# Optimization experiments

Measured on AMD Instinct MI355X. Metric: run time of the kernel, lower is better.

The kernel has to match this reference:

```python
import jax, jax.numpy as jnp
import numpy as np

B, H, W, C = 16, 64, 64, 192
NH, WS, SHIFT = 6, 8, 4          # heads, window size, shift (window//2)
DEPTH, MLP_R = 2, 4
N = WS * WS                      # tokens per window = 64
HD = C // NH                     # head dim = 32
SCALE = HD ** -0.5
TBL = (2 * WS - 1) ** 2          # relative-bias table size = 225
NW = (H // WS) * (W // WS)       # windows per image = 64


def _rel_pos_index():
    coords = np.stack(np.meshgrid(np.arange(WS), np.arange(WS), indexing='ij')).reshape(2, -1)
    rel = (coords[:, :, None] - coords[:, None, :]).transpose(1, 2, 0)
    rel[..., 0] += WS - 1
    rel[..., 1] += WS - 1
    rel[..., 0] *= 2 * WS - 1
    return jnp.asarray(rel.sum(-1))  # [N, N] int


def _attn_mask():
    # Swin shifted-window mask: region ids then pairwise -100 where ids differ.
    img = np.zeros((H, W))
    sl = (slice(0, -WS), slice(-WS, -SHIFT), slice(-SHIFT, None))
    cnt = 0
    for hs in sl:
        for ws in sl:
            img[hs, ws] = cnt
            cnt += 1
    mw = img.reshape(H // WS, WS, W // WS, WS).transpose(0, 2, 1, 3).reshape(-1, N)
    diff = mw[:, None, :] - mw[:, :, None]
    return jnp.asarray(np.where(diff != 0, -100.0, 0.0).astype(np.float32))  # [NW, N, N]


REL_IDX = _rel_pos_index()
ATTN_MASK = _attn_mask()


def _ln(x, g, b, eps=1e-5):
    mu = x.mean(-1, keepdims=True)
    var = ((x - mu) ** 2).mean(-1, keepdims=True)
    return (x - mu) * jax.lax.rsqrt(var + eps) * g + b


def setup_inputs() -> dict:
    key = jax.random.key(0)
    ks = jax.random.split(key, 8)
    s = 0.02
    return {
        'x': jax.random.normal(ks[0], (B, H * W, C), jnp.float32),
        'norm1_g': jnp.ones((DEPTH, C)), 'norm1_b': jnp.zeros((DEPTH, C)),
        'qkv_w': jax.random.normal(ks[1], (DEPTH, 3 * C, C)) * s,
        'qkv_b': jnp.zeros((DEPTH, 3 * C)),
        'bias_table': jax.random.normal(ks[2], (DEPTH, TBL, NH)) * s,
        'proj_w': jax.random.normal(ks[3], (DEPTH, C, C)) * s,
        'proj_b': jnp.zeros((DEPTH, C)),
        'norm2_g': jnp.ones((DEPTH, C)), 'norm2_b': jnp.zeros((DEPTH, C)),
        'fc1_w': jax.random.normal(ks[4], (DEPTH, MLP_R * C, C)) * s,
        'fc1_b': jnp.zeros((DEPTH, MLP_R * C)),
        'fc2_w': jax.random.normal(ks[5], (DEPTH, C, MLP_R * C)) * s,
        'fc2_b': jnp.zeros((DEPTH, C)),
    }


def _block(x, shift, n1g, n1b, qw, qb, tbl, pw, pb, n2g, n2b, f1w, f1b, f2w, f2b):
    shortcut = x
    y = _ln(x, n1g, n1b).reshape(B, H, W, C)
    if shift > 0:
        y = jnp.roll(y, (-shift, -shift), axis=(1, 2))
    # window partition -> [B*NW, N, C]
    win = y.reshape(B, H // WS, WS, W // WS, WS, C).transpose(0, 1, 3, 2, 4, 5).reshape(-1, N, C)
    qkv = (win @ qw.T + qb).reshape(-1, N, 3, NH, HD).transpose(2, 0, 3, 1, 4)
    q, k, v = qkv[0] * SCALE, qkv[1], qkv[2]          # each [B*NW, NH, N, HD]
    attn = jnp.einsum('bhnd,bhmd->bhnm', q, k)
    attn = attn + tbl[REL_IDX].transpose(2, 0, 1)[None]  # relative position bias
    if shift > 0:
        attn = (attn.reshape(B, NW, NH, N, N) + ATTN_MASK[None, :, None]).reshape(-1, NH, N, N)
    attn = jax.nn.softmax(attn, axis=-1)
    o = jnp.einsum('bhnm,bhmd->bhnd', attn, v).transpose(0, 2, 1, 3).reshape(-1, N, C)
    o = o @ pw.T + pb
    # window reverse
    y = o.reshape(B, H // WS, W // WS, WS, WS, C).transpose(0, 1, 3, 2, 4, 5).reshape(B, H, W, C)
    if shift > 0:
        y = jnp.roll(y, (shift, shift), axis=(1, 2))
    x = shortcut + y.reshape(B, H * W, C)
    h = _ln(x, n2g, n2b)
    h = jax.nn.gelu(h @ f1w.T + f1b, approximate=False)  # torch nn.GELU = exact erf
    return x + (h @ f2w.T + f2b)


def reference(x, norm1_g, norm1_b, qkv_w, qkv_b, bias_table, proj_w, proj_b,
              norm2_g, norm2_b, fc1_w, fc1_b, fc2_w, fc2_b):
    for i in range(DEPTH):
        shift = 0 if i % 2 == 0 else SHIFT
        x = _block(x, shift, norm1_g[i], norm1_b[i], qkv_w[i], qkv_b[i], bias_table[i],
                   proj_w[i], proj_b[i], norm2_g[i], norm2_b[i],
                   fc1_w[i], fc1_b[i], fc2_w[i], fc2_b[i])
    return x
```

## Files before the change

### kernel.cpp

```cpp
#include <hip/hip_runtime.h>
#include <hip/hip_bf16.h>
#include <math.h>

typedef __hip_bfloat16 bf16;
typedef short bf16x8 __attribute__((ext_vector_type(8)));
typedef short s16x4 __attribute__((ext_vector_type(4)));
typedef float f32x4 __attribute__((ext_vector_type(4)));

#define TOKENS 65536
#define C_ 192

__device__ __forceinline__ float b2f(bf16 v){ return __bfloat162float(v); }
__device__ __forceinline__ bf16 f2b(float v){ return __float2bfloat16(v); }
__device__ __forceinline__ short f2s(float v){
  bf16 b = __float2bfloat16(v);
  union { bf16 b; short s; } u; u.b = b; return u.s;
}
__device__ __forceinline__ float s2f(short s){
  union { unsigned u; float f; } c; c.u = ((unsigned)(unsigned short)s) << 16; return c.f;
}

__global__ void detect_k(const unsigned* __restrict__ g, int* __restrict__ flag){
  *flag = (g[0] == 0x3F800000u) ? 1 : 0;
}
__global__ void xconv_k(const void* __restrict__ x, float* __restrict__ y, int n,
                        const int* __restrict__ flag){
  int i = blockIdx.x*blockDim.x + threadIdx.x;
  if (i >= n) return;
  if (*flag) y[i] = ((const float*)x)[i];
  else       y[i] = b2f(((const bf16*)x)[i]);
}
struct WPtrs { const void* p[13]; };
__global__ void wconv_all_k(WPtrs wp, const int* __restrict__ offs, const int* __restrict__ lens,
                            bf16* __restrict__ dst, int total, const int* __restrict__ flag){
  int i = blockIdx.x*blockDim.x + threadIdx.x;
  if (i >= total) return;
  int t = 0;
  while (t < 12 && i >= offs[t+1]) t++;
  int j = i - offs[t];
  if (j >= lens[t]) return;
  if (*flag) dst[i] = f2b(((const float*)wp.p[t])[j]);
  else       dst[i] = ((const bf16*)wp.p[t])[j];
}
__global__ void outconv_k(const float* __restrict__ x, void* __restrict__ y, int n,
                          const int* __restrict__ flag){
  int i = blockIdx.x*blockDim.x + threadIdx.x;
  if (i >= n) return;
  if (*flag) ((float*)y)[i] = x[i];
  else       ((bf16*)y)[i]  = f2b(x[i]);
}

__global__ void bias_setup_k(const bf16* __restrict__ bt, float* __restrict__ biasF){
  int idx = blockIdx.x*blockDim.x + threadIdx.x;
  if (idx >= 2*6*64*64) return;
  int v = idx & 63;
  int lane = (idx >> 6) & 63;
  int rest = idx >> 12;
  int head = rest % 6, dd = rest / 6;
  int jt = v >> 4, it = (v >> 2) & 3, r = v & 3;
  int quad = lane >> 4, lr = lane & 15;
  int j = jt*16 + quad*4 + r;
  int i = it*16 + lr;
  int rel = ((i>>3) - (j>>3) + 7)*15 + ((i&7) - (j&7) + 7);
  biasF[idx] = b2f(bt[(dd*225 + rel)*6 + head]);
}

__global__ void mlp_repack_k(const bf16* __restrict__ f1w, const bf16* __restrict__ f2w,
                             bf16* __restrict__ w1p, bf16* __restrict__ w2p){
  int id = blockIdx.x*blockDim.x + threadIdx.x;
  if (id >= 589824) return;
  int arr = id / 294912;
  int r = id % 294912;
  int d = r / 147456;
  int e = r % 147456;
  int j = e & 7, lane = (e >> 3) & 63, frag = e >> 9;
  int lr = lane & 15, quad = lane >> 4;
  if (arr == 0){
    int ks = frag % 6, t = frag / 6;
    int mh = t & 1, cc = t >> 1;
    w1p[(size_t)d*147456 + e] =
        f1w[(size_t)d*147456 + (size_t)(cc*32 + mh*16 + lr)*192 + ks*32 + quad*8 + j];
  } else {
    int ct = frag % 12, cc = frag / 12;
    w2p[(size_t)d*147456 + e] =
        f2w[(size_t)d*147456 + (size_t)(ct*16 + lr)*768 + cc*32 + quad*8 + j];
  }
}

__global__ __launch_bounds__(768, 1) void attn_fused_k(float* __restrict__ xres,
    const bf16* __restrict__ n1g, const bf16* __restrict__ n1b,
    const bf16* __restrict__ qw, const bf16* __restrict__ qb,
    const bf16* __restrict__ pw, const bf16* __restrict__ pb,
    const float* __restrict__ biasF, int shift)
{
  extern __shared__ char smem[];
  short* xo = (short*)smem;
  int win = blockIdx.x;
  int tid = threadIdx.x;
  int wave = tid >> 6, lane = tid & 63;
  int quad = lane >> 4, lr = lane & 15;
  int head = wave >> 1, half = wave & 1;
  int b_ = win >> 6, wl = win & 63, wh = wl >> 3, wwi = wl & 7;
  short* kh  = (short*)(smem + 25600 + head*17408);
  short* vth = kh + 2048;
  short* qP  = vth + 2304;

  int c0 = lane*3;
  float g0 = b2f(n1g[c0]), g1 = b2f(n1g[c0+1]), g2 = b2f(n1g[c0+2]);
  float e0 = b2f(n1b[c0]), e1 = b2f(n1b[c0+1]), e2 = b2f(n1b[c0+2]);
  #pragma unroll
  for (int p = 0; p < 6; p++){
    int tok = p*12 + wave;
    if (tok < 64){
      int hh = (wh*8 + (tok>>3) + shift) & 63, ww = (wwi*8 + (tok&7) + shift) & 63;
      const float* rowp = xres + ((size_t)(b_<<12) + (hh<<6) + ww)*C_;
      float v0 = rowp[c0], v1 = rowp[c0+1], v2 = rowp[c0+2];
      float s = v0+v1+v2;
      #pragma unroll
      for (int off=32; off; off>>=1) s += __shfl_xor(s, off);
      float mu = s * (1.0f/192.0f);
      float d0=v0-mu, d1=v1-mu, d2=v2-mu;
      float q = d0*d0+d1*d1+d2*d2;
      #pragma unroll
      for (int off=32; off; off>>=1) q += __shfl_xor(q, off);
      float rstd = rsqrtf(q*(1.0f/192.0f) + 1e-5f);
      xo[tok*200 + c0]   = f2s(d0*rstd*g0 + e0);
      xo[tok*200 + c0+1] = f2s(d1*rstd*g1 + e1);
      xo[tok*200 + c0+2] = f2s(d2*rstd*g2 + e2);
    }
  }
  __syncthreads();

  const short* qwd = (const short*)qw;
  #pragma unroll
  for (int cc = 0; cc < 3; cc++){
    int nbase = cc*192 + head*32;
    f32x4 acc[2][2];
    #pragma unroll
    for (int mt = 0; mt < 2; mt++)
      #pragma unroll
      for (int nt = 0; nt < 2; nt++) acc[mt][nt] = (f32x4){0.f,0.f,0.f,0.f};
    #pragma unroll
    for (int ks = 0; ks < 6; ks++){
      bf16x8 af[2], bx[2];
      #pragma unroll
      for (int mt = 0; mt < 2; mt++)
        af[mt] = *(const bf16x8*)(qwd + (size_t)(nbase + mt*16 + lr)*192 + ks*32 + quad*8);
      #pragma unroll
      for (int nt = 0; nt < 2; nt++)
        bx[nt] = *(const bf16x8*)&xo[((2*half + nt)*16 + lr)*200 + ks*32 + quad*8];
      #pragma unroll
      for (int mt = 0; mt < 2; mt++)
        #pragma unroll
        for (int nt = 0; nt < 2; nt++)
          acc[mt][nt] = __builtin_amdgcn_mfma_f32_16x16x32_bf16(af[mt], bx[nt], acc[mt][nt], 0, 0, 0);
    }
    #pragma unroll
    for (int mt = 0; mt < 2; mt++){
      float bv[4];
      #pragma unroll
      for (int r = 0; r < 4; r++) bv[r] = b2f(qb[nbase + mt*16 + quad*4 + r]);
      #pragma unroll
      for (int nt = 0; nt < 2; nt++){
        int tok = (2*half + nt)*16 + lr;
        if (cc == 0){
          s16x4 pk;
          #pragma unroll
          for (int r = 0; r < 4; r++) pk[r] = f2s((acc[mt][nt][r] + bv[r]) * 0.17677669529663689f);
          *(s16x4*)&qP[tok*32 + mt*16 + quad*4] = pk;
        } else if (cc == 1){
          s16x4 pk;
          #pragma unroll
          for (int r = 0; r < 4; r++) pk[r] = f2s(acc[mt][nt][r] + bv[r]);
          *(s16x4*)&kh[tok*32 + mt*16 + quad*4] = pk;
        } else {
          #pragma unroll
          for (int r = 0; r < 4; r++)
            vth[(mt*16 + quad*4 + r)*72 + tok] = f2s(acc[mt][nt][r] + bv[r]);
        }
      }
    }
  }
  __syncthreads();

  bf16x8 ak[4], bq[2];
  #pragma unroll
  for (int jt = 0; jt < 4; jt++) ak[jt] = *(const bf16x8*)&kh[(jt*16 + lr)*32 + quad*8];
  #pragma unroll
  for (int it = 0; it < 2; it++)
    bq[it] = *(const bf16x8*)&qP[((2*half + it)*16 + lr)*32 + quad*8];
  __syncthreads();

  f32x4 S[4][2];
  #pragma unroll
  for (int jt = 0; jt < 4; jt++)
    #pragma unroll
    for (int it = 0; it < 2; it++) S[jt][it] = (f32x4){0.f,0.f,0.f,0.f};
  #pragma unroll
  for (int jt = 0; jt < 4; jt++)
    #pragma unroll
    for (int it = 0; it < 2; it++)
      S[jt][it] = __builtin_amdgcn_mfma_f32_16x16x32_bf16(ak[jt], bq[it], S[jt][it], 0, 0, 0);

  const f32x4* bm = (const f32x4*)(biasF + ((size_t)head*64 + lane)*64);
  #pragma unroll
  for (int jt = 0; jt < 4; jt++)
    #pragma unroll
    for (int it = 0; it < 2; it++) S[jt][it] += bm[jt*4 + 2*half + it];

  if (shift){
    int idi[2];
    #pragma unroll
    for (int it = 0; it < 2; it++){
      int itg = 2*half + it;
      int hh = wh*8 + itg*2 + (lr >> 3);
      int wwc = wwi*8 + (lr & 7);
      idi[it] = (hh < 56 ? 0 : (hh < 60 ? 1 : 2))*3 + (wwc < 56 ? 0 : (wwc < 60 ? 1 : 2));
    }
    #pragma unroll
    for (int jt = 0; jt < 4; jt++)
      #pragma unroll
      for (int r = 0; r < 4; r++){
        int j = jt*16 + quad*4 + r;
        int hh = wh*8 + (j >> 3), wwc = wwi*8 + (j & 7);
        int idj = (hh < 56 ? 0 : (hh < 60 ? 1 : 2))*3 + (wwc < 56 ? 0 : (wwc < 60 ? 1 : 2));
        #pragma unroll
        for (int it = 0; it < 2; it++)
          if (idj != idi[it]) S[jt][it][r] -= 100.f;
      }
  }
  #pragma unroll
  for (int it = 0; it < 2; it++){
    float m = -1e30f;
    #pragma unroll
    for (int jt = 0; jt < 4; jt++)
      #pragma unroll
      for (int r = 0; r < 4; r++) m = fmaxf(m, S[jt][it][r]);
    m = fmaxf(m, __shfl_xor(m, 16));
    m = fmaxf(m, __shfl_xor(m, 32));
    float s = 0.f;
    #pragma unroll
    for (int jt = 0; jt < 4; jt++)
      #pragma unroll
      for (int r = 0; r < 4; r++){
        float e = __expf(S[jt][it][r] - m);
        S[jt][it][r] = e; s += e;
      }
    s += __shfl_xor(s, 16);
    s += __shfl_xor(s, 32);
    float inv = 1.0f / s;
    #pragma unroll
    for (int jt = 0; jt < 4; jt++){
      s16x4 pk;
      #pragma unroll
      for (int r = 0; r < 4; r++) pk[r] = f2s(S[jt][it][r] * inv);
      *(s16x4*)&qP[((2*half + it)*16 + lr)*68 + jt*16 + quad*4] = pk;
    }
  }
  __syncthreads();

  bf16x8 va[2][2], pv[2][2];
  #pragma unroll
  for (int mt = 0; mt < 2; mt++)
    #pragma unroll
    for (int ks = 0; ks < 2; ks++)
      va[mt][ks] = *(const bf16x8*)&vth[(mt*16 + lr)*72 + ks*32 + quad*8];
  #pragma unroll
  for (int nt = 0; nt < 2; nt++)
    #pragma unroll
    for (int ks = 0; ks < 2; ks++)
      pv[nt][ks] = *(const bf16x8*)&qP[((2*half + nt)*16 + lr)*68 + ks*32 + quad*8];

  f32x4 O[2][2];
  #pragma unroll
  for (int mt = 0; mt < 2; mt++)
    #pragma unroll
    for (int nt = 0; nt < 2; nt++) O[mt][nt] = (f32x4){0.f,0.f,0.f,0.f};
  #pragma unroll
  for (int mt = 0; mt < 2; mt++)
    #pragma unroll
    for (int nt = 0; nt < 2; nt++)
      #pragma unroll
      for (int ks = 0; ks < 2; ks++)
        O[mt][nt] = __builtin_amdgcn_mfma_f32_16x16x32_bf16(va[mt][ks], pv[nt][ks], O[mt][nt], 0, 0, 0);

  #pragma unroll
  for (int mt = 0; mt < 2; mt++)
    #pragma unroll
    for (int nt = 0; nt < 2; nt++){
      s16x4 pk;
      #pragma unroll
      for (int r = 0; r < 4; r++) pk[r] = f2s(O[mt][nt][r]);
      *(s16x4*)&xo[((2*half + nt)*16 + lr)*200 + head*32 + mt*16 + quad*4] = pk;
    }
  __syncthreads();

  int wm = wave / 6, wn = wave % 6;
  f32x4 po[2][2];
  #pragma unroll
  for (int mt = 0; mt < 2; mt++)
    #pragma unroll
    for (int nt = 0; nt < 2; nt++) po[mt][nt] = (f32x4){0.f,0.f,0.f,0.f};
  const short* pwd = (const short*)pw;
  #pragma unroll
  for (int ks = 0; ks < 6; ks++){
    bf16x8 ao[2], bw[2];
    #pragma unroll
    for (int mt = 0; mt < 2; mt++)
      ao[mt] = *(const bf16x8*)&xo[(wm*32 + mt*16 + lr)*200 + ks*32 + quad*8];
    #pragma unroll
    for (int nt = 0; nt < 2; nt++)
      bw[nt] = *(const bf16x8*)(pwd + (size_t)(wn*32 + nt*16 + lr)*192 + ks*32 + quad*8);
    #pragma unroll
    for (int mt = 0; mt < 2; mt++)
      #pragma unroll
      for (int nt = 0; nt < 2; nt++)
        po[mt][nt] = __builtin_amdgcn_mfma_f32_16x16x32_bf16(ao[mt], bw[nt], po[mt][nt], 0, 0, 0);
  }
  #pragma unroll
  for (int nt = 0; nt < 2; nt++){
    int n = wn*32 + nt*16 + lr;
    float bv = b2f(pb[n]);
    #pragma unroll
    for (int mt = 0; mt < 2; mt++){
      #pragma unroll
      for (int r = 0; r < 4; r++){
        int tok = wm*32 + mt*16 + quad*4 + r;
        int hh = (wh*8 + (tok>>3) + shift) & 63, ww = (wwi*8 + (tok&7) + shift) & 63;
        float* dst = xres + ((size_t)(b_<<12) + (hh<<6) + ww)*C_ + n;
        *dst += po[mt][nt][r] + bv;
      }
    }
  }
}

__global__ __launch_bounds__(256, 2) void mlp_direct_k(float* __restrict__ xres,
    const bf16* __restrict__ n2g, const bf16* __restrict__ n2b,
    const bf16* __restrict__ w1p, const bf16* __restrict__ f1b,
    const bf16* __restrict__ w2p, const bf16* __restrict__ f2bv)
{
  __shared__ short HsAll[4][32*36];
  int tid = threadIdx.x;
  int wave = tid >> 6, lane = tid & 63;
  int quad = lane >> 4, lr = lane & 15;
  short* Hs = HsAll[wave];
  int t0 = blockIdx.x*128 + wave*32;

  bf16x8 xh[2][6];
  #pragma unroll
  for (int nt = 0; nt < 2; nt++){
    const float* rowp = xres + (size_t)(t0 + nt*16 + lr)*C_;
    float v[6][8];
    float s = 0.f;
    #pragma unroll
    for (int ks = 0; ks < 6; ks++){
      int cb = ks*32 + quad*8;
      #pragma unroll
      for (int j = 0; j < 8; j++){ v[ks][j] = rowp[cb+j]; s += v[ks][j]; }
    }
    s += __shfl_xor(s, 16); s += __shfl_xor(s, 32);
    float mu = s*(1.0f/192.0f);
    float q = 0.f;
    #pragma unroll
    for (int ks = 0; ks < 6; ks++)
      #pragma unroll
      for (int j = 0; j < 8; j++){ float d = v[ks][j]-mu; q += d*d; }
    q += __shfl_xor(q, 16); q += __shfl_xor(q, 32);
    float rstd = rsqrtf(q*(1.0f/192.0f) + 1e-5f);
    #pragma unroll
    for (int ks = 0; ks < 6; ks++){
      int cb = ks*32 + quad*8;
      #pragma unroll
      for (int j = 0; j < 8; j++)
        xh[nt][ks][j] = f2s((v[ks][j]-mu)*rstd*b2f(n2g[cb+j]) + b2f(n2b[cb+j]));
    }
  }

  f32x4 acc[12][2];
  #pragma unroll
  for (int ct = 0; ct < 12; ct++)
    #pragma unroll
    for (int nt = 0; nt < 2; nt++) acc[ct][nt] = (f32x4){0.f,0.f,0.f,0.f};

  const short* w1 = (const short*)w1p;
  const short* w2 = (const short*)w2p;

  for (int cc = 0; cc < 24; cc++){
    f32x4 hacc[2][2];
    #pragma unroll
    for (int mh = 0; mh < 2; mh++)
      #pragma unroll
      for (int nt = 0; nt < 2; nt++) hacc[mh][nt] = (f32x4){0.f,0.f,0.f,0.f};
    #pragma unroll
    for (int ks = 0; ks < 6; ks++){
      bf16x8 af0 = *(const bf16x8*)(w1 + (size_t)(cc*12 + ks)*512 + lane*8);
      bf16x8 af1 = *(const bf16x8*)(w1 + (size_t)(cc*12 + 6 + ks)*512 + lane*8);
      hacc[0][0] = __builtin_amdgcn_mfma_f32_16x16x32_bf16(af0, xh[0][ks], hacc[0][0], 0, 0, 0);
      hacc[0][1] = __builtin_amdgcn_mfma_f32_16x16x32_bf16(af0, xh[1][ks], hacc[0][1], 0, 0, 0);
      hacc[1][0] = __builtin_amdgcn_mfma_f32_16x16x32_bf16(af1, xh[0][ks], hacc[1][0], 0, 0, 0);
      hacc[1][1] = __builtin_amdgcn_mfma_f32_16x16x32_bf16(af1, xh[1][ks], hacc[1][1], 0, 0, 0);
    }
    #pragma unroll
    for (int mh = 0; mh < 2; mh++){
      s16x4 bb = *(const s16x4*)((const short*)f1b + cc*32 + mh*16 + quad*4);
      #pragma unroll
      for (int nt = 0; nt < 2; nt++){
        s16x4 pk;
        #pragma unroll
        for (int r = 0; r < 4; r++){
          float x = hacc[mh][nt][r] + s2f(bb[r]);
          float y = x*(0.7978845608f + 0.0356774081f*x*x);
          float t = __expf(2.0f*fminf(y, 9.0f));
          pk[r] = f2s(x*t/(t + 1.0f));
        }
        *(s16x4*)&Hs[(nt*16 + lr)*36 + mh*16 + quad*4] = pk;
      }
    }
    bf16x8 ah0 = *(const bf16x8*)&Hs[lr*36 + quad*8];
    bf16x8 ah1 = *(const bf16x8*)&Hs[(16 + lr)*36 + quad*8];
    #pragma unroll
    for (int ct = 0; ct < 12; ct++){
      bf16x8 bw = *(const bf16x8*)(w2 + (size_t)(cc*12 + ct)*512 + lane*8);
      acc[ct][0] = __builtin_amdgcn_mfma_f32_16x16x32_bf16(ah0, bw, acc[ct][0], 0, 0, 0);
      acc[ct][1] = __builtin_amdgcn_mfma_f32_16x16x32_bf16(ah1, bw, acc[ct][1], 0, 0, 0);
    }
  }

  #pragma unroll
  for (int ct = 0; ct < 12; ct++){
    int n = ct*16 + lr;
    float bv = b2f(f2bv[n]);
    #pragma unroll
    for (int nt = 0; nt < 2; nt++)
      #pragma unroll
      for (int r = 0; r < 4; r++){
        int m = t0 + nt*16 + quad*4 + r;
        xres[(size_t)m*C_ + n] += acc[ct][nt][r] + bv;
      }
  }
}

extern "C" void kernel_launch(void* const* d_in, const int* in_sizes, int n_in,
                              void* d_out, int out_size, void* d_ws, size_t ws_size,
                              hipStream_t stream)
{
  (void)in_sizes; (void)n_in; (void)out_size;

  if (ws_size < (size_t)52117000) return;
  char* ws = (char*)d_ws;
  float* xf   = (float*)ws;
  bf16* canon = (bf16*)(ws + 50331648);
  int*  flagp = (int*)(ws + 52116608);
  float* biasF = (float*)d_out;
  bf16* w1p = (bf16*)((char*)d_out + 196608);
  bf16* w2p = (bf16*)((char*)d_out + 786432);

  static const int W_OFF[13] = {0, 384, 768, 221952, 223104, 225856, 299584,
                                299968, 300352, 300736, 595648, 597184, 892096};
  const int W_TOTAL = 892480;

  hipFuncSetAttribute((const void*)attn_fused_k,
                      hipFuncAttributeMaxDynamicSharedMemorySize, 130048);

  detect_k<<<1, 1, 0, stream>>>((const unsigned*)d_in[1], flagp);

  WPtrs wp;
  for (int i = 0; i < 13; i++) wp.p[i] = d_in[i+1];
  {
    int* meta = (int*)(ws + 52116672);
    struct Init {
      static __global__ void run(int* meta){
        const int offs[13] = {0, 384, 768, 221952, 223104, 225856, 299584,
                              299968, 300352, 300736, 595648, 597184, 892096};
        const int lens[13] = {384, 384, 221184, 1152, 2700, 73728, 384,
                              384, 384, 294912, 1536, 294912, 384};
        int i = threadIdx.x;
        if (i < 13){ meta[i] = offs[i]; meta[13+i] = lens[i]; }
      }
    };
    hipLaunchKernelGGL(Init::run, dim3(1), dim3(16), 0, stream, meta);
    wconv_all_k<<<(W_TOTAL + 255)/256, 256, 0, stream>>>(wp, meta, meta+13, canon, W_TOTAL, flagp);
  }

  const int nelem = TOKENS*C_;
  xconv_k<<<nelem/256, 256, 0, stream>>>(d_in[0], xf, nelem, flagp);

  const bf16* n1g = canon + W_OFF[0];
  const bf16* n1b = canon + W_OFF[1];
  const bf16* qw  = canon + W_OFF[2];
  const bf16* qb  = canon + W_OFF[3];
  const bf16* bt  = canon + W_OFF[4];
  const bf16* pw  = canon + W_OFF[5];
  const bf16* pb  = canon + W_OFF[6];
  const bf16* n2g = canon + W_OFF[7];
  const bf16* n2b = canon + W_OFF[8];
  const bf16* f1w = canon + W_OFF[9];
  const bf16* f1b = canon + W_OFF[10];
  const bf16* f2w = canon + W_OFF[11];
  const bf16* f2bv= canon + W_OFF[12];

  bias_setup_k<<<(2*6*64*64)/256, 256, 0, stream>>>(bt, biasF);
  mlp_repack_k<<<(589824 + 255)/256, 256, 0, stream>>>(f1w, f2w, w1p, w2p);

  for (int d = 0; d < 2; d++){
    int shift = d ? 4 : 0;
    attn_fused_k<<<1024, 768, 130048, stream>>>(xf,
        n1g + d*192, n1b + d*192, qw + d*576*192, qb + d*576,
        pw + d*192*192, pb + d*192, biasF + d*6*64*64, shift);
    mlp_direct_k<<<512, 256, 0, stream>>>(xf,
        n2g + d*192, n2b + d*192, w1p + d*147456, f1b + d*768,
        w2p + d*147456, f2bv + d*192);
  }
  outconv_k<<<nelem/256, 256, 0, stream>>>(xf, d_out, nelem, flagp);
}
```

Baseline: 574.7 us.

## Pass Q and P fragments via lane shuffles instead of shared memory

The Q tile and the softmax probability tile are no longer written to and read back from shared memory. They stay in registers and are rearranged into the MFMA B-operand layout with cross-lane shuffles. This drops the per-head qP scratch region and two barriers, which shrinks dynamic LDS from about 127KB to 76KB and could allow more than one 768-thread block per CU (launch bounds raised to 6). The cost is extra shuffle instructions and higher register pressure, and the larger launch-bounds hint may force spills.

```diff
diff --git a/kernel.cpp b/kernel.cpp
--- a/kernel.cpp
+++ b/kernel.cpp
@@ -18,6 +18,13 @@
 }
 __device__ __forceinline__ float s2f(short s){
   union { unsigned u; float f; } c; c.u = ((unsigned)(unsigned short)s) << 16; return c.f;
+}
+__device__ __forceinline__ s16x4 shfl64(s16x4 v, int src){
+  union { s16x4 v; int i[2]; } a, b;
+  a.v = v;
+  b.i[0] = __shfl(a.i[0], src);
+  b.i[1] = __shfl(a.i[1], src);
+  return b.v;
 }
 
 __global__ void detect_k(const unsigned* __restrict__ g, int* __restrict__ flag){
@@ -87,7 +94,7 @@
   }
 }
 
-__global__ __launch_bounds__(768, 1) void attn_fused_k(float* __restrict__ xres,
+__global__ __launch_bounds__(768, 6) void attn_fused_k(float* __restrict__ xres,
     const bf16* __restrict__ n1g, const bf16* __restrict__ n1b,
     const bf16* __restrict__ qw, const bf16* __restrict__ qb,
     const bf16* __restrict__ pw, const bf16* __restrict__ pb,
@@ -101,9 +108,12 @@
   int quad = lane >> 4, lr = lane & 15;
   int head = wave >> 1, half = wave & 1;
   int b_ = win >> 6, wl = win & 63, wh = wl >> 3, wwi = wl & 7;
-  short* kh  = (short*)(smem + 25600 + head*17408);
+  short* kh  = (short*)(smem + 25600 + head*8704);
   short* vth = kh + 2048;
-  short* qP  = vth + 2304;
+
+  int src_lo = ((lane >> 4) & 1)*32 + lr;
+  int src_hi = src_lo + 16;
+  int hi_half = (lane >> 5) & 1;
 
   int c0 = lane*3;
   float g0 = b2f(n1g[c0]), g1 = b2f(n1g[c0+1]), g2 = b2f(n1g[c0+2]);
@@ -131,6 +141,7 @@
   }
   __syncthreads();
 
+  s16x4 qpk[2][2];
   const short* qwd = (const short*)qw;
   #pragma unroll
   for (int cc = 0; cc < 3; cc++){
@@ -167,7 +178,7 @@
           s16x4 pk;
           #pragma unroll
           for (int r = 0; r < 4; r++) pk[r] = f2s((acc[mt][nt][r] + bv[r]) * 0.17677669529663689f);
-          *(s16x4*)&qP[tok*32 + mt*16 + quad*4] = pk;
+          qpk[mt][nt] = pk;
         } else if (cc == 1){
           s16x4 pk;
           #pragma unroll
@@ -187,9 +198,15 @@
   #pragma unroll
   for (int jt = 0; jt < 4; jt++) ak[jt] = *(const bf16x8*)&kh[(jt*16 + lr)*32 + quad*8];
   #pragma unroll
-  for (int it = 0; it < 2; it++)
-    bq[it] = *(const bf16x8*)&qP[((2*half + it)*16 + lr)*32 + quad*8];
-  __syncthreads();
+  for (int it = 0; it < 2; it++){
+    s16x4 val = hi_half ? qpk[1][it] : qpk[0][it];
+    s16x4 lo = shfl64(val, src_lo);
+    s16x4 hi = shfl64(val, src_hi);
+    bf16x8 b;
+    #pragma unroll
+    for (int r = 0; r < 4; r++){ b[r] = lo[r]; b[4+r] = hi[r]; }
+    bq[it] = b;
+  }
 
   f32x4 S[4][2];
   #pragma unroll
@@ -229,6 +246,8 @@
           if (idj != idi[it]) S[jt][it][r] -= 100.f;
       }
   }
+
+  bf16x8 pv[2][2];
   #pragma unroll
   for (int it = 0; it < 2; it++){
     float m = -1e30f;
@@ -249,27 +268,32 @@
     s += __shfl_xor(s, 16);
     s += __shfl_xor(s, 32);
     float inv = 1.0f / s;
+    s16x4 pkj[4];
     #pragma unroll
     for (int jt = 0; jt < 4; jt++){
       s16x4 pk;
       #pragma unroll
       for (int r = 0; r < 4; r++) pk[r] = f2s(S[jt][it][r] * inv);
-      *(s16x4*)&qP[((2*half + it)*16 + lr)*68 + jt*16 + quad*4] = pk;
-    }
-  }
-  __syncthreads();
-
-  bf16x8 va[2][2], pv[2][2];
+      pkj[jt] = pk;
+    }
+    #pragma unroll
+    for (int ks = 0; ks < 2; ks++){
+      s16x4 val = hi_half ? pkj[2*ks + 1] : pkj[2*ks];
+      s16x4 lo = shfl64(val, src_lo);
+      s16x4 hi = shfl64(val, src_hi);
+      bf16x8 b;
+      #pragma unroll
+      for (int r = 0; r < 4; r++){ b[r] = lo[r]; b[4+r] = hi[r]; }
+      pv[it][ks] = b;
+    }
+  }
+
+  bf16x8 va[2][2];
   #pragma unroll
   for (int mt = 0; mt < 2; mt++)
     #pragma unroll
     for (int ks = 0; ks < 2; ks++)
       va[mt][ks] = *(const bf16x8*)&vth[(mt*16 + lr)*72 + ks*32 + quad*8];
-  #pragma unroll
-  for (int nt = 0; nt < 2; nt++)
-    #pragma unroll
-    for (int ks = 0; ks < 2; ks++)
-      pv[nt][ks] = *(const bf16x8*)&qP[((2*half + nt)*16 + lr)*68 + ks*32 + quad*8];
 
   f32x4 O[2][2];
   #pragma unroll
@@ -460,7 +484,7 @@
   const int W_TOTAL = 892480;
 
   hipFuncSetAttribute((const void*)attn_fused_k,
-                      hipFuncAttributeMaxDynamicSharedMemorySize, 130048);
+                      hipFuncAttributeMaxDynamicSharedMemorySize, 77824);
 
   detect_k<<<1, 1, 0, stream>>>((const unsigned*)d_in[1], flagp);
 
@@ -504,7 +528,7 @@
 
   for (int d = 0; d < 2; d++){
     int shift = d ? 4 : 0;
-    attn_fused_k<<<1024, 768, 130048, stream>>>(xf,
+    attn_fused_k<<<1024, 768, 77824, stream>>>(xf,
         n1g + d*192, n1b + d*192, qw + d*576*192, qb + d*576,
         pw + d*192*192, pb + d*192, biasF + d*6*64*64, shift);
     mlp_direct_k<<<512, 256, 0, stream>>>(xf,
```

Result: slower. 607.5 us (+5.7%).

## Halve MLP tokens per wave to raise occupancy and vectorize residual update

Applied to the files above, without the earlier changes.

The fused MLP kernel now handles 16 tokens per wave instead of 32, which halves the accumulator registers. Launch bounds go from 2 to 4 blocks per SM and the grid doubles to 1024 blocks. The second GEMM swaps its MFMA operand order so each lane holds 4 consecutive output channels of one token. That lets the residual add use 16-byte vector loads and stores. The cost is that each wave reads the weights from global/L2 twice as often per token, since weight reuse across token tiles is halved.

```diff
diff --git a/kernel.cpp b/kernel.cpp
--- a/kernel.cpp
+++ b/kernel.cpp
@@ -334,22 +334,21 @@
   }
 }
 
-__global__ __launch_bounds__(256, 2) void mlp_direct_k(float* __restrict__ xres,
+__global__ __launch_bounds__(256, 4) void mlp_tlp_k(float* __restrict__ xres,
     const bf16* __restrict__ n2g, const bf16* __restrict__ n2b,
     const bf16* __restrict__ w1p, const bf16* __restrict__ f1b,
     const bf16* __restrict__ w2p, const bf16* __restrict__ f2bv)
 {
-  __shared__ short HsAll[4][32*36];
+  __shared__ short HsAll[4][16*36];
   int tid = threadIdx.x;
   int wave = tid >> 6, lane = tid & 63;
   int quad = lane >> 4, lr = lane & 15;
   short* Hs = HsAll[wave];
-  int t0 = blockIdx.x*128 + wave*32;
-
-  bf16x8 xh[2][6];
-  #pragma unroll
-  for (int nt = 0; nt < 2; nt++){
-    const float* rowp = xres + (size_t)(t0 + nt*16 + lr)*C_;
+  int t0 = blockIdx.x*64 + wave*16;
+
+  bf16x8 xh[6];
+  {
+    const float* rowp = xres + (size_t)(t0 + lr)*C_;
     float v[6][8];
     float s = 0.f;
     #pragma unroll
@@ -372,71 +371,62 @@
       int cb = ks*32 + quad*8;
       #pragma unroll
       for (int j = 0; j < 8; j++)
-        xh[nt][ks][j] = f2s((v[ks][j]-mu)*rstd*b2f(n2g[cb+j]) + b2f(n2b[cb+j]));
-    }
-  }
-
-  f32x4 acc[12][2];
-  #pragma unroll
-  for (int ct = 0; ct < 12; ct++)
-    #pragma unroll
-    for (int nt = 0; nt < 2; nt++) acc[ct][nt] = (f32x4){0.f,0.f,0.f,0.f};
+        xh[ks][j] = f2s((v[ks][j]-mu)*rstd*b2f(n2g[cb+j]) + b2f(n2b[cb+j]));
+    }
+  }
+
+  f32x4 acc[12];
+  #pragma unroll
+  for (int ct = 0; ct < 12; ct++) acc[ct] = (f32x4){0.f,0.f,0.f,0.f};
 
   const short* w1 = (const short*)w1p;
   const short* w2 = (const short*)w2p;
 
   for (int cc = 0; cc < 24; cc++){
-    f32x4 hacc[2][2];
-    #pragma unroll
-    for (int mh = 0; mh < 2; mh++)
-      #pragma unroll
-      for (int nt = 0; nt < 2; nt++) hacc[mh][nt] = (f32x4){0.f,0.f,0.f,0.f};
+    f32x4 hacc[2];
+    hacc[0] = (f32x4){0.f,0.f,0.f,0.f};
+    hacc[1] = (f32x4){0.f,0.f,0.f,0.f};
     #pragma unroll
     for (int ks = 0; ks < 6; ks++){
       bf16x8 af0 = *(const bf16x8*)(w1 + (size_t)(cc*12 + ks)*512 + lane*8);
       bf16x8 af1 = *(const bf16x8*)(w1 + (size_t)(cc*12 + 6 + ks)*512 + lane*8);
-      hacc[0][0] = __builtin_amdgcn_mfma_f32_16x16x32_bf16(af0, xh[0][ks], hacc[0][0], 0, 0, 0);
-      hacc[0][1] = __builtin_amdgcn_mfma_f32_16x16x32_bf16(af0, xh[1][ks], hacc[0][1], 0, 0, 0);
-      hacc[1][0] = __builtin_amdgcn_mfma_f32_16x16x32_bf16(af1, xh[0][ks], hacc[1][0], 0, 0, 0);
-      hacc[1][1] = __builtin_amdgcn_mfma_f32_16x16x32_bf16(af1, xh[1][ks], hacc[1][1], 0, 0, 0);
+      hacc[0] = __builtin_amdgcn_mfma_f32_16x16x32_bf16(af0, xh[ks], hacc[0], 0, 0, 0);
+      hacc[1] = __builtin_amdgcn_mfma_f32_16x16x32_bf16(af1, xh[ks], hacc[1], 0, 0, 0);
     }
     #pragma unroll
     for (int mh = 0; mh < 2; mh++){
       s16x4 bb = *(const s16x4*)((const short*)f1b + cc*32 + mh*16 + quad*4);
-      #pragma unroll
-      for (int nt = 0; nt < 2; nt++){
-        s16x4 pk;
-        #pragma unroll
-        for (int r = 0; r < 4; r++){
-          float x = hacc[mh][nt][r] + s2f(bb[r]);
-          float y = x*(0.7978845608f + 0.0356774081f*x*x);
-          float t = __expf(2.0f*fminf(y, 9.0f));
-          pk[r] = f2s(x*t/(t + 1.0f));
-        }
-        *(s16x4*)&Hs[(nt*16 + lr)*36 + mh*16 + quad*4] = pk;
+      s16x4 pk;
+      #pragma unroll
+      for (int r = 0; r < 4; r++){
+        float x = hacc[mh][r] + s2f(bb[r]);
+        float y = x*(0.7978845608f + 0.0356774081f*x*x);
+        float t = __expf(2.0f*fminf(y, 9.0f));
+        pk[r] = f2s(x*t/(t + 1.0f));
       }
-    }
-    bf16x8 ah0 = *(const bf16x8*)&Hs[lr*36 + quad*8];
-    bf16x8 ah1 = *(const bf16x8*)&Hs[(16 + lr)*36 + quad*8];
+      *(s16x4*)&Hs[lr*36 + mh*16 + quad*4] = pk;
+    }
+    bf16x8 ah = *(const bf16x8*)&Hs[lr*36 + quad*8];
     #pragma unroll
     for (int ct = 0; ct < 12; ct++){
       bf16x8 bw = *(const bf16x8*)(w2 + (size_t)(cc*12 + ct)*512 + lane*8);
-      acc[ct][0] = __builtin_amdgcn_mfma_f32_16x16x32_bf16(ah0, bw, acc[ct][0], 0, 0, 0);
-      acc[ct][1] = __builtin_amdgcn_mfma_f32_16x16x32_bf16(ah1, bw, acc[ct][1], 0, 0, 0);
-    }
-  }
-
-  #pragma unroll
-  for (int ct = 0; ct < 12; ct++){
-    int n = ct*16 + lr;
-    float bv = b2f(f2bv[n]);
-    #pragma unroll
-    for (int nt = 0; nt < 2; nt++)
-      #pragma unroll
-      for (int r = 0; r < 4; r++){
-        int m = t0 + nt*16 + quad*4 + r;
-        xres[(size_t)m*C_ + n] += acc[ct][nt][r] + bv;
-      }
+      acc[ct] = __builtin_amdgcn_mfma_f32_16x16x32_bf16(bw, ah, acc[ct], 0, 0, 0);
+    }
+  }
+
+  {
+    int m = t0 + lr;
+    float* rowd = xres + (size_t)m*C_;
+    #pragma unroll
+    for (int ct = 0; ct < 12; ct++){
+      int n0 = ct*16 + quad*4;
+      s16x4 bb = *(const s16x4*)((const short*)f2bv + n0);
+      f32x4* dst = (f32x4*)(rowd + n0);
+      f32x4 cur = *dst;
+      #pragma unroll
+      for (int r = 0; r < 4; r++) cur[r] += acc[ct][r] + s2f(bb[r]);
+      *dst = cur;
+    }
   }
 }
 
@@ -507,7 +497,7 @@
     attn_fused_k<<<1024, 768, 130048, stream>>>(xf,
         n1g + d*192, n1b + d*192, qw + d*576*192, qb + d*576,
         pw + d*192*192, pb + d*192, biasF + d*6*64*64, shift);
-    mlp_direct_k<<<512, 256, 0, stream>>>(xf,
+    mlp_tlp_k<<<1024, 256, 0, stream>>>(xf,
         n2g + d*192, n2b + d*192, w1p + d*147456, f1b + d*768,
         w2p + d*147456, f2bv + d*192);
   }
```

New measurement: 629.9 us. 1.1x slower.
